# Optimization experiments

Hardware: AMD Instinct MI355X
Metric: run time of the kernel (lower is better)

Reference implementation:

```python
import jax, jax.numpy as jnp
import numpy as np

TOP_K = 2

def setup_inputs() -> dict:
    key = jax.random.key(0)
    k1, k2 = jax.random.split(key)
    hidden_states = jax.random.normal(k1, (4, 4096, 4096), dtype=jnp.float32)
    # nn.Linear(dim, num_experts, bias=False) weight: [num_experts, dim]
    router_weight = jax.random.normal(k2, (64, 4096), dtype=jnp.float32) * (4096 ** -0.5)
    return {"hidden_states": hidden_states, "router_weight": router_weight}

def reference(hidden_states, router_weight):
    # logits: (batch, seq, num_experts)
    logits = jnp.einsum('bsd,ed->bse', hidden_states, router_weight)
    # Shazeer et al. 2017 Eq. 1: softmax over the kept top-k logits.
    topk_logits, topk_indices = jax.lax.top_k(logits, TOP_K)
    topk_scores = jax.nn.softmax(topk_logits, axis=-1)  # (batch, seq, top_k)
    return topk_scores, topk_indices
```

## Files before the change

### kernel.cpp

```cpp
#include <hip/hip_runtime.h>
#include <math.h>

#define TOKENS 16384
#define DIM    4096
#define NEXP   64
#define KSPLIT 4
#define KSLICE (DIM / KSPLIT)
#define BK     32
#define NCHUNK (KSLICE / BK)
#define NCHUNK_G (DIM / BK)

typedef _Float16 f16x8 __attribute__((ext_vector_type(8)));
typedef float    f32x4 __attribute__((ext_vector_type(4)));

#define MFMA16(a, b, c) __builtin_amdgcn_mfma_f32_16x16x32_f16((a), (b), (c), 0, 0, 0)

__device__ __forceinline__ void gload16(const void* g, void* l) {
    __builtin_amdgcn_global_load_lds(
        (const __attribute__((address_space(1))) void*)g,
        (__attribute__((address_space(3))) void*)l, 16, 0, 0);
}

__global__ __launch_bounds__(256)
void pack_w_kernel(const float* __restrict__ w, uint4* __restrict__ wpk) {
    const int lane = threadIdx.x & 63;
    const int t    = threadIdx.x >> 6;
    const int c    = blockIdx.x;
    const int e    = 16 * t + (lane & 15);
    const int k0   = 32 * c + 8 * (lane >> 4);

    const float* src = w + (size_t)e * DIM + k0;
    const float4 v0 = *(const float4*)(src);
    const float4 v1 = *(const float4*)(src + 4);
    const float xs[8] = {v0.x, v0.y, v0.z, v0.w, v1.x, v1.y, v1.z, v1.w};

    f16x8 hi, lo;
#pragma unroll
    for (int j = 0; j < 8; ++j) {
        const float xv = xs[j];
        _Float16 h = (_Float16)xv;
        float hf = (float)h;
        if (fabsf(xv) < 6.103515625e-05f) {
            h = (_Float16)0.f; hf = 0.f;
        }
        hi[j] = h;
        lo[j] = (_Float16)((xv - hf) * 65536.f);
    }

    wpk[(size_t)c * 512 + (2 * t + 0) * 64 + lane] = *(const uint4*)&hi;
    wpk[(size_t)c * 512 + (2 * t + 1) * 64 + lane] = *(const uint4*)&lo;
}

__device__ __forceinline__ void split_a(const f32x4 lo, const f32x4 hi,
                                        f16x8& ah, f16x8& al) {
    const float xs[8] = {lo[0], lo[1], lo[2], lo[3], hi[0], hi[1], hi[2], hi[3]};
#pragma unroll
    for (int j = 0; j < 8; ++j) {
        const float xv = xs[j];
        const _Float16 h = (_Float16)xv;
        ah[j] = h;
        al[j] = (_Float16)((xv - (float)h) * 65536.f);
    }
}

__device__ __forceinline__ void fma3(const f16x8 ah, const f16x8 al,
                                     const f16x8 bh, const f16x8 bl,
                                     f32x4& a1, f32x4& a2) {
    a1 = MFMA16(ah, bh, a1);
    a2 = MFMA16(ah, bl, a2);
    a2 = MFMA16(al, bh, a2);
}

__global__ __launch_bounds__(256)
__attribute__((amdgpu_waves_per_eu(4, 4)))
void router_gemm_kernel(const float* __restrict__ x,
                        const uint4* __restrict__ wpk,
                        float* __restrict__ part) {
    __shared__ uint4 lds[2048];

    const int tid  = threadIdx.x;
    const int lane = tid & 63;
    const int wv   = tid >> 6;
    const int bid  = blockIdx.x;
    const int ks   = bid & (KSPLIT - 1);
    const int tb   = bid >> 2;
    const int wt0  = tb * 64 + wv * 16;

    const int rl = lane >> 3;
    const int sb = (lane & 7) ^ rl;
    const float* xsrc0 = x + (size_t)(wt0 + rl)     * DIM + ks * KSLICE + 4 * sb;
    const float* xsrc1 = x + (size_t)(wt0 + 8 + rl) * DIM + ks * KSLICE + 4 * sb;
    const uint4* bsrc = wpk + (size_t)(ks * NCHUNK) * 512 + (2 * wv) * 64 + lane;

    const int r  = lane & 15;
    const int kb = 2 * (lane >> 4);
    const int xi0 = r * 8 + ((kb    ) ^ (r & 7));
    const int xi1 = r * 8 + ((kb + 1) ^ (r & 7));

    f32x4 a10, a11, a12, a13, a20, a21, a22, a23;
    const f32x4 zero = {0.f, 0.f, 0.f, 0.f};
    a10 = a11 = a12 = a13 = zero;
    a20 = a21 = a22 = a23 = zero;

    auto STAGE = [&](int cc, int bsel) {
        uint4* Xb = &lds[bsel * 1024 + wv * 128];
        uint4* Bb = &lds[bsel * 1024 + 512 + (2 * wv) * 64];
        gload16(xsrc0 + cc * BK,            Xb);
        gload16(xsrc1 + cc * BK,            Xb + 64);
        gload16(bsrc + (size_t)cc * 512,      Bb);
        gload16(bsrc + (size_t)cc * 512 + 64, Bb + 64);
    };

    STAGE(0, 0);

#pragma unroll 1
    for (int c = 0; c < NCHUNK; ++c) {
        STAGE((c + 1) & (NCHUNK - 1), (c + 1) & 1);

        asm volatile("s_waitcnt vmcnt(4)" ::: "memory");
        __builtin_amdgcn_s_barrier();

        const uint4* Xr = &lds[(c & 1) * 1024 + wv * 128];
        const uint4* Br = &lds[(c & 1) * 1024 + 512];

        const f32x4 xlo = *(const f32x4*)&Xr[xi0];
        const f32x4 xhi = *(const f32x4*)&Xr[xi1];
        const f16x8 bh0 = *(const f16x8*)&Br[0 * 64 + lane];
        const f16x8 bl0 = *(const f16x8*)&Br[1 * 64 + lane];
        const f16x8 bh1 = *(const f16x8*)&Br[2 * 64 + lane];
        const f16x8 bl1 = *(const f16x8*)&Br[3 * 64 + lane];
        const f16x8 bh2 = *(const f16x8*)&Br[4 * 64 + lane];
        const f16x8 bl2 = *(const f16x8*)&Br[5 * 64 + lane];
        const f16x8 bh3 = *(const f16x8*)&Br[6 * 64 + lane];
        const f16x8 bl3 = *(const f16x8*)&Br[7 * 64 + lane];

        f16x8 ah, al;
        split_a(xlo, xhi, ah, al);
        fma3(ah, al, bh0, bl0, a10, a20);
        fma3(ah, al, bh1, bl1, a11, a21);
        fma3(ah, al, bh2, bl2, a12, a22);
        fma3(ah, al, bh3, bl3, a13, a23);

        asm volatile("s_waitcnt lgkmcnt(0)" ::: "memory");
        __builtin_amdgcn_s_barrier();
    }

    float* pout = part + ((size_t)ks * TOKENS + wt0 + 4 * (lane >> 4)) * NEXP
                + (lane & 15);
    const f32x4 v0 = a10 + a20 * (1.f / 65536.f);
    const f32x4 v1 = a11 + a21 * (1.f / 65536.f);
    const f32x4 v2 = a12 + a22 * (1.f / 65536.f);
    const f32x4 v3 = a13 + a23 * (1.f / 65536.f);
#pragma unroll
    for (int rr = 0; rr < 4; ++rr) {
        pout[(size_t)rr * NEXP +  0] = v0[rr];
        pout[(size_t)rr * NEXP + 16] = v1[rr];
        pout[(size_t)rr * NEXP + 32] = v2[rr];
        pout[(size_t)rr * NEXP + 48] = v3[rr];
    }
}

__global__ __launch_bounds__(256)
void topk_kernel(const float* __restrict__ part, float* __restrict__ out) {
    const int lane  = threadIdx.x & 63;
    const int wv    = threadIdx.x >> 6;
    const int token = blockIdx.x * 4 + wv;

    float logit = 0.f;
#pragma unroll
    for (int s = 0; s < KSPLIT; ++s)
        logit += part[((size_t)s * TOKENS + token) * NEXP + lane];

    float v1 = logit; int i1 = lane;
#pragma unroll
    for (int off = 32; off > 0; off >>= 1) {
        const float ov = __shfl_xor(v1, off);
        const int   oi = __shfl_xor(i1, off);
        if (ov > v1 || (ov == v1 && oi < i1)) { v1 = ov; i1 = oi; }
    }
    float v2 = (lane == i1) ? -INFINITY : logit; int i2 = lane;
#pragma unroll
    for (int off = 32; off > 0; off >>= 1) {
        const float ov = __shfl_xor(v2, off);
        const int   oi = __shfl_xor(i2, off);
        if (ov > v2 || (ov == v2 && oi < i2)) { v2 = ov; i2 = oi; }
    }

    if (lane == 0) {
        const float e = expf(v2 - v1);
        const float r = 1.f / (1.f + e);
        out[2 * token + 0] = r;
        out[2 * token + 1] = e * r;
        out[2 * TOKENS + 2 * token + 0] = (float)i1;
        out[2 * TOKENS + 2 * token + 1] = (float)i2;
    }
}

extern "C" void kernel_launch(void* const* d_in, const int* in_sizes, int n_in,
                              void* d_out, int out_size, void* d_ws, size_t ws_size,
                              hipStream_t stream) {
    const float* x = (const float*)d_in[0];
    const float* w = (const float*)d_in[1];
    float* out  = (float*)d_out;
    float* part = (float*)d_ws;
    uint4* wpk = (uint4*)((char*)d_ws + (size_t)KSPLIT * TOKENS * NEXP * sizeof(float));

    pack_w_kernel<<<NCHUNK_G, 256, 0, stream>>>(w, wpk);
    router_gemm_kernel<<<(TOKENS / 64) * KSPLIT, 256, 0, stream>>>(x, wpk, part);
    topk_kernel<<<TOKENS / 4, 256, 0, stream>>>(part, out);
}
```

Before: 380.3 us.

## Load activations directly to registers and stage weights in 8-chunk LDS blocks

The router GEMM no longer routes activation tiles through LDS. Each lane loads its fp32 activations straight into registers, with a software pipeline that prefetches two chunks ahead. Weight tiles are staged into LDS eight K-chunks at a time, so a barrier is needed only once per eight chunks instead of twice per chunk. Blocks grow to 512 threads covering 128 tokens, the waves-per-EU attribute is removed, and sched_barriers pin the ordering of loads and MFMAs. The intent is to cut barrier and LDS round-trip overhead on this memory-bound kernel, at the cost of more registers and exposed latency whenever a weight block is restaged.

Measured after the change: 393.1 us. 1.03x slower.

```diff
diff --git a/kernel.cpp b/kernel.cpp
--- a/kernel.cpp
+++ b/kernel.cpp
@@ -8,12 +8,15 @@
 #define KSLICE (DIM / KSPLIT)
 #define BK     32
 #define NCHUNK (KSLICE / BK)
+#define QCHUNK 8
+#define TB     128
 #define NCHUNK_G (DIM / BK)
 
 typedef _Float16 f16x8 __attribute__((ext_vector_type(8)));
 typedef float    f32x4 __attribute__((ext_vector_type(4)));
 
 #define MFMA16(a, b, c) __builtin_amdgcn_mfma_f32_16x16x32_f16((a), (b), (c), 0, 0, 0)
+#define SBAR() __builtin_amdgcn_sched_barrier(0)
 
 __device__ __forceinline__ void gload16(const void* g, void* l) {
     __builtin_amdgcn_global_load_lds(
@@ -51,9 +54,9 @@
     wpk[(size_t)c * 512 + (2 * t + 1) * 64 + lane] = *(const uint4*)&lo;
 }
 
-__device__ __forceinline__ void split_a(const f32x4 lo, const f32x4 hi,
+__device__ __forceinline__ void split_a(const float4 lo, const float4 hi,
                                         f16x8& ah, f16x8& al) {
-    const float xs[8] = {lo[0], lo[1], lo[2], lo[3], hi[0], hi[1], hi[2], hi[3]};
+    const float xs[8] = {lo.x, lo.y, lo.z, lo.w, hi.x, hi.y, hi.z, hi.w};
 #pragma unroll
     for (int j = 0; j < 8; ++j) {
         const float xv = xs[j];
@@ -71,78 +74,85 @@
     a2 = MFMA16(al, bh, a2);
 }
 
-__global__ __launch_bounds__(256)
-__attribute__((amdgpu_waves_per_eu(4, 4)))
+__global__ __launch_bounds__(512)
 void router_gemm_kernel(const float* __restrict__ x,
                         const uint4* __restrict__ wpk,
                         float* __restrict__ part) {
-    __shared__ uint4 lds[2048];
+    __shared__ uint4 Blds[QCHUNK * 512];
 
     const int tid  = threadIdx.x;
     const int lane = tid & 63;
     const int wv   = tid >> 6;
     const int bid  = blockIdx.x;
     const int ks   = bid & (KSPLIT - 1);
-    const int tb   = bid >> 2;
-    const int wt0  = tb * 64 + wv * 16;
-
-    const int rl = lane >> 3;
-    const int sb = (lane & 7) ^ rl;
-    const float* xsrc0 = x + (size_t)(wt0 + rl)     * DIM + ks * KSLICE + 4 * sb;
-    const float* xsrc1 = x + (size_t)(wt0 + 8 + rl) * DIM + ks * KSLICE + 4 * sb;
-    const uint4* bsrc = wpk + (size_t)(ks * NCHUNK) * 512 + (2 * wv) * 64 + lane;
-
-    const int r  = lane & 15;
-    const int kb = 2 * (lane >> 4);
-    const int xi0 = r * 8 + ((kb    ) ^ (r & 7));
-    const int xi1 = r * 8 + ((kb + 1) ^ (r & 7));
+    const int wt0  = (bid >> 2) * TB + wv * 16;
+
+    const float* xp = x + (size_t)(wt0 + (lane & 15)) * DIM
+                    + ks * KSLICE + 8 * (lane >> 4);
+
+    const uint4* bsl = wpk + (size_t)ks * NCHUNK * 512 + (size_t)(wv * 8) * 64 + lane;
+
+    auto STAGE_B = [&](int q) {
+        const uint4* src = bsl + (size_t)q * QCHUNK * 512;
+#pragma unroll
+        for (int i = 0; i < 8; ++i)
+            gload16(src + i * 64, &Blds[(wv * 8 + i) * 64]);
+    };
 
     f32x4 a10, a11, a12, a13, a20, a21, a22, a23;
     const f32x4 zero = {0.f, 0.f, 0.f, 0.f};
     a10 = a11 = a12 = a13 = zero;
     a20 = a21 = a22 = a23 = zero;
 
-    auto STAGE = [&](int cc, int bsel) {
-        uint4* Xb = &lds[bsel * 1024 + wv * 128];
-        uint4* Bb = &lds[bsel * 1024 + 512 + (2 * wv) * 64];
-        gload16(xsrc0 + cc * BK,            Xb);
-        gload16(xsrc1 + cc * BK,            Xb + 64);
-        gload16(bsrc + (size_t)cc * 512,      Bb);
-        gload16(bsrc + (size_t)cc * 512 + 64, Bb + 64);
-    };
-
-    STAGE(0, 0);
+    float4 rl[4], rh[4];
+
+    STAGE_B(0);
+    rl[0] = *(const float4*)(xp);
+    rh[0] = *(const float4*)(xp + 4);
+    rl[1] = *(const float4*)(xp + BK);
+    rh[1] = *(const float4*)(xp + BK + 4);
+    asm volatile("s_waitcnt vmcnt(0)" ::: "memory");
+    __builtin_amdgcn_s_barrier();
 
 #pragma unroll 1
-    for (int c = 0; c < NCHUNK; ++c) {
-        STAGE((c + 1) & (NCHUNK - 1), (c + 1) & 1);
-
-        asm volatile("s_waitcnt vmcnt(4)" ::: "memory");
-        __builtin_amdgcn_s_barrier();
-
-        const uint4* Xr = &lds[(c & 1) * 1024 + wv * 128];
-        const uint4* Br = &lds[(c & 1) * 1024 + 512];
-
-        const f32x4 xlo = *(const f32x4*)&Xr[xi0];
-        const f32x4 xhi = *(const f32x4*)&Xr[xi1];
-        const f16x8 bh0 = *(const f16x8*)&Br[0 * 64 + lane];
-        const f16x8 bl0 = *(const f16x8*)&Br[1 * 64 + lane];
-        const f16x8 bh1 = *(const f16x8*)&Br[2 * 64 + lane];
-        const f16x8 bl1 = *(const f16x8*)&Br[3 * 64 + lane];
-        const f16x8 bh2 = *(const f16x8*)&Br[4 * 64 + lane];
-        const f16x8 bl2 = *(const f16x8*)&Br[5 * 64 + lane];
-        const f16x8 bh3 = *(const f16x8*)&Br[6 * 64 + lane];
-        const f16x8 bl3 = *(const f16x8*)&Br[7 * 64 + lane];
-
-        f16x8 ah, al;
-        split_a(xlo, xhi, ah, al);
-        fma3(ah, al, bh0, bl0, a10, a20);
-        fma3(ah, al, bh1, bl1, a11, a21);
-        fma3(ah, al, bh2, bl2, a12, a22);
-        fma3(ah, al, bh3, bl3, a13, a23);
-
-        asm volatile("s_waitcnt lgkmcnt(0)" ::: "memory");
-        __builtin_amdgcn_s_barrier();
+    for (int c = 0; c < NCHUNK; c += 4) {
+        if (c && (c & (QCHUNK - 1)) == 0) {
+            asm volatile("s_waitcnt lgkmcnt(0)" ::: "memory");
+            __builtin_amdgcn_s_barrier();
+            STAGE_B(c >> 3);
+            asm volatile("s_waitcnt vmcnt(0)" ::: "memory");
+            __builtin_amdgcn_s_barrier();
+        }
+#pragma unroll
+        for (int u = 0; u < 4; ++u) {
+            const int cc = c + u;
+            SBAR();
+            {
+                const int cn = (cc + 2) & (NCHUNK - 1);
+                rl[(u + 2) & 3] = *(const float4*)(xp + cn * BK);
+                rh[(u + 2) & 3] = *(const float4*)(xp + cn * BK + 4);
+            }
+            SBAR();
+            const uint4* Br = &Blds[((cc & (QCHUNK - 1)) * 8) * 64];
+            f16x8 ah, al;
+            split_a(rl[u], rh[u], ah, al);
+            {
+                const f16x8 bh0 = *(const f16x8*)&Br[0 * 64 + lane];
+                const f16x8 bl0 = *(const f16x8*)&Br[1 * 64 + lane];
+                const f16x8 bh1 = *(const f16x8*)&Br[2 * 64 + lane];
+                const f16x8 bl1 = *(const f16x8*)&Br[3 * 64 + lane];
+                fma3(ah, al, bh0, bl0, a10, a20);
+                fma3(ah, al, bh1, bl1, a11, a21);
+            }
+            {
+                const f16x8 bh2 = *(const f16x8*)&Br[4 * 64 + lane];
+                const f16x8 bl2 = *(const f16x8*)&Br[5 * 64 + lane];
+                const f16x8 bh3 = *(const f16x8*)&Br[6 * 64 + lane];
+                const f16x8 bl3 = *(const f16x8*)&Br[7 * 64 + lane];
+                fma3(ah, al, bh2, bl2, a12, a22);
+                fma3(ah, al, bh3, bl3, a13, a23);
+            }
+        }
     }
 
     float* pout = part + ((size_t)ks * TOKENS + wt0 + 4 * (lane >> 4)) * NEXP
@@ -206,6 +216,6 @@
     uint4* wpk = (uint4*)((char*)d_ws + (size_t)KSPLIT * TOKENS * NEXP * sizeof(float));
 
     pack_w_kernel<<<NCHUNK_G, 256, 0, stream>>>(w, wpk);
-    router_gemm_kernel<<<(TOKENS / 64) * KSPLIT, 256, 0, stream>>>(x, wpk, part);
+    router_gemm_kernel<<<(TOKENS / TB) * KSPLIT, 512, 0, stream>>>(x, wpk, part);
     topk_kernel<<<TOKENS / 4, 256, 0, stream>>>(part, out);
 }
```

## Enlarge GEMM block to 128 tokens with 2x2 wave tiling and deeper X prefetch

Applied to the files above, without the earlier changes.

The router GEMM block grows from 256 to 512 threads and covers 128 tokens. Each wave now computes a 32-token by 32-expert tile, so the f16 hi/lo split of activations is shared across two expert tiles and each weight fragment is reused across two token tiles. X is prefetched two chunks ahead into a 4-deep LDS ring, and MFMA priority is raised with s_setprio. The aim is to cut redundant split work and hide global load latency better. The cost is more LDS, more registers per wave, and half as many blocks, which may hurt occupancy and load balance.

Result: no change. 385.2 us (+1.3%).

```diff
diff --git a/kernel.cpp b/kernel.cpp
--- a/kernel.cpp
+++ b/kernel.cpp
@@ -8,6 +8,7 @@
 #define KSLICE (DIM / KSPLIT)
 #define BK     32
 #define NCHUNK (KSLICE / BK)
+#define TB     128
 #define NCHUNK_G (DIM / BK)
 
 typedef _Float16 f16x8 __attribute__((ext_vector_type(8)));
@@ -71,92 +72,109 @@
     a2 = MFMA16(al, bh, a2);
 }
 
-__global__ __launch_bounds__(256)
+__global__ __launch_bounds__(512)
 __attribute__((amdgpu_waves_per_eu(4, 4)))
 void router_gemm_kernel(const float* __restrict__ x,
                         const uint4* __restrict__ wpk,
                         float* __restrict__ part) {
-    __shared__ uint4 lds[2048];
+    __shared__ uint4 lds[5120];
 
     const int tid  = threadIdx.x;
     const int lane = tid & 63;
     const int wv   = tid >> 6;
+    const int tf   = wv >> 1;
+    const int et   = wv & 1;
     const int bid  = blockIdx.x;
     const int ks   = bid & (KSPLIT - 1);
-    const int tb   = bid >> 2;
-    const int wt0  = tb * 64 + wv * 16;
+    const int token0 = (bid >> 2) * TB;
 
     const int rl = lane >> 3;
     const int sb = (lane & 7) ^ rl;
-    const float* xsrc0 = x + (size_t)(wt0 + rl)     * DIM + ks * KSLICE + 4 * sb;
-    const float* xsrc1 = x + (size_t)(wt0 + 8 + rl) * DIM + ks * KSLICE + 4 * sb;
-    const uint4* bsrc = wpk + (size_t)(ks * NCHUNK) * 512 + (2 * wv) * 64 + lane;
-
-    const int r  = lane & 15;
-    const int kb = 2 * (lane >> 4);
-    const int xi0 = r * 8 + ((kb    ) ^ (r & 7));
-    const int xi1 = r * 8 + ((kb + 1) ^ (r & 7));
-
-    f32x4 a10, a11, a12, a13, a20, a21, a22, a23;
+    const float* xsrc0 = x + (size_t)(token0 + 16 * wv + rl) * DIM
+                       + ks * KSLICE + 4 * sb;
+    const float* xsrc1 = xsrc0 + (size_t)8 * DIM;
+    const uint4* bsrc = wpk + (size_t)(ks * NCHUNK) * 512 + wv * 64 + lane;
+
+    const int xib = ((lane >> 3) & 1) * 64 + (lane & 7) * 8;
+    const int xk0 = (2 * (lane >> 4)    ) ^ (lane & 7);
+    const int xk1 = (2 * (lane >> 4) + 1) ^ (lane & 7);
+
+    f32x4 a1[2][2], a2[2][2];
     const f32x4 zero = {0.f, 0.f, 0.f, 0.f};
-    a10 = a11 = a12 = a13 = zero;
-    a20 = a21 = a22 = a23 = zero;
-
-    auto STAGE = [&](int cc, int bsel) {
-        uint4* Xb = &lds[bsel * 1024 + wv * 128];
-        uint4* Bb = &lds[bsel * 1024 + 512 + (2 * wv) * 64];
-        gload16(xsrc0 + cc * BK,            Xb);
-        gload16(xsrc1 + cc * BK,            Xb + 64);
-        gload16(bsrc + (size_t)cc * 512,      Bb);
-        gload16(bsrc + (size_t)cc * 512 + 64, Bb + 64);
-    };
-
-    STAGE(0, 0);
+#pragma unroll
+    for (int f = 0; f < 2; ++f)
+#pragma unroll
+        for (int e = 0; e < 2; ++e) { a1[f][e] = zero; a2[f][e] = zero; }
+
+    gload16(xsrc0,          &lds[0 * 1024 + wv * 128]);
+    gload16(xsrc0 + BK,     &lds[1 * 1024 + wv * 128]);
+    gload16(xsrc1,          &lds[0 * 1024 + wv * 128 + 64]);
+    gload16(xsrc1 + BK,     &lds[1 * 1024 + wv * 128 + 64]);
+    gload16(bsrc,           &lds[4096 + 0 * 512 + wv * 64]);
 
 #pragma unroll 1
     for (int c = 0; c < NCHUNK; ++c) {
-        STAGE((c + 1) & (NCHUNK - 1), (c + 1) & 1);
-
-        asm volatile("s_waitcnt vmcnt(4)" ::: "memory");
+        {
+            const int cb = (c + 1) & (NCHUNK - 1);
+            gload16(bsrc + (size_t)cb * 512,
+                    &lds[4096 + ((c + 1) & 1) * 512 + wv * 64]);
+        }
+        if (!(c & 1)) {
+            const int c2 = (c + 2) & (NCHUNK - 1);
+            const int c3 = (c + 3) & (NCHUNK - 1);
+            uint4* d2 = &lds[((c + 2) & 3) * 1024 + wv * 128];
+            uint4* d3 = &lds[((c + 3) & 3) * 1024 + wv * 128];
+            gload16(xsrc0 + c2 * BK, d2);
+            gload16(xsrc0 + c3 * BK, d3);
+            gload16(xsrc1 + c2 * BK, d2 + 64);
+            gload16(xsrc1 + c3 * BK, d3 + 64);
+        }
+        asm volatile("s_waitcnt vmcnt(5)" ::: "memory");
         __builtin_amdgcn_s_barrier();
 
-        const uint4* Xr = &lds[(c & 1) * 1024 + wv * 128];
-        const uint4* Br = &lds[(c & 1) * 1024 + 512];
-
-        const f32x4 xlo = *(const f32x4*)&Xr[xi0];
-        const f32x4 xhi = *(const f32x4*)&Xr[xi1];
-        const f16x8 bh0 = *(const f16x8*)&Br[0 * 64 + lane];
-        const f16x8 bl0 = *(const f16x8*)&Br[1 * 64 + lane];
-        const f16x8 bh1 = *(const f16x8*)&Br[2 * 64 + lane];
-        const f16x8 bl1 = *(const f16x8*)&Br[3 * 64 + lane];
-        const f16x8 bh2 = *(const f16x8*)&Br[4 * 64 + lane];
-        const f16x8 bl2 = *(const f16x8*)&Br[5 * 64 + lane];
-        const f16x8 bh3 = *(const f16x8*)&Br[6 * 64 + lane];
-        const f16x8 bl3 = *(const f16x8*)&Br[7 * 64 + lane];
-
-        f16x8 ah, al;
-        split_a(xlo, xhi, ah, al);
-        fma3(ah, al, bh0, bl0, a10, a20);
-        fma3(ah, al, bh1, bl1, a11, a21);
-        fma3(ah, al, bh2, bl2, a12, a22);
-        fma3(ah, al, bh3, bl3, a13, a23);
+        const uint4* Xr = &lds[(c & 3) * 1024];
+        const uint4* Br = &lds[4096 + (c & 1) * 512];
+
+        f16x8 ah0, al0, ah1, al1;
+        {
+            const int b0 = (2 * tf + 0) * 128 + xib;
+            const int b1 = (2 * tf + 1) * 128 + xib;
+            const f32x4 A0l = *(const f32x4*)&Xr[b0 + xk0];
+            const f32x4 A0h = *(const f32x4*)&Xr[b0 + xk1];
+            const f32x4 A1l = *(const f32x4*)&Xr[b1 + xk0];
+            const f32x4 A1h = *(const f32x4*)&Xr[b1 + xk1];
+            split_a(A0l, A0h, ah0, al0);
+            split_a(A1l, A1h, ah1, al1);
+        }
+        const f16x8 bh0 = *(const f16x8*)&Br[(4 * et + 0) * 64 + lane];
+        const f16x8 bl0 = *(const f16x8*)&Br[(4 * et + 1) * 64 + lane];
+        const f16x8 bh1 = *(const f16x8*)&Br[(4 * et + 2) * 64 + lane];
+        const f16x8 bl1 = *(const f16x8*)&Br[(4 * et + 3) * 64 + lane];
+
+        __builtin_amdgcn_s_setprio(1);
+        fma3(ah0, al0, bh0, bl0, a1[0][0], a2[0][0]);
+        fma3(ah0, al0, bh1, bl1, a1[0][1], a2[0][1]);
+        fma3(ah1, al1, bh0, bl0, a1[1][0], a2[1][0]);
+        fma3(ah1, al1, bh1, bl1, a1[1][1], a2[1][1]);
+        __builtin_amdgcn_s_setprio(0);
 
         asm volatile("s_waitcnt lgkmcnt(0)" ::: "memory");
         __builtin_amdgcn_s_barrier();
     }
 
-    float* pout = part + ((size_t)ks * TOKENS + wt0 + 4 * (lane >> 4)) * NEXP
-                + (lane & 15);
-    const f32x4 v0 = a10 + a20 * (1.f / 65536.f);
-    const f32x4 v1 = a11 + a21 * (1.f / 65536.f);
-    const f32x4 v2 = a12 + a22 * (1.f / 65536.f);
-    const f32x4 v3 = a13 + a23 * (1.f / 65536.f);
-#pragma unroll
-    for (int rr = 0; rr < 4; ++rr) {
-        pout[(size_t)rr * NEXP +  0] = v0[rr];
-        pout[(size_t)rr * NEXP + 16] = v1[rr];
-        pout[(size_t)rr * NEXP + 32] = v2[rr];
-        pout[(size_t)rr * NEXP + 48] = v3[rr];
+#pragma unroll
+    for (int f = 0; f < 2; ++f) {
+#pragma unroll
+        for (int e = 0; e < 2; ++e) {
+            const f32x4 v = a1[f][e] + a2[f][e] * (1.f / 65536.f);
+            float* pout = part
+                + ((size_t)ks * TOKENS + token0 + (2 * tf + f) * 16
+                   + 4 * (lane >> 4)) * NEXP
+                + 16 * (2 * et + e) + (lane & 15);
+#pragma unroll
+            for (int rr = 0; rr < 4; ++rr)
+                pout[(size_t)rr * NEXP] = v[rr];
+        }
     }
 }
 
@@ -206,6 +224,6 @@
     uint4* wpk = (uint4*)((char*)d_ws + (size_t)KSPLIT * TOKENS * NEXP * sizeof(float));
 
     pack_w_kernel<<<NCHUNK_G, 256, 0, stream>>>(w, wpk);
-    router_gemm_kernel<<<(TOKENS / 64) * KSPLIT, 256, 0, stream>>>(x, wpk, part);
+    router_gemm_kernel<<<(TOKENS / TB) * KSPLIT, 512, 0, stream>>>(x, wpk, part);
     topk_kernel<<<TOKENS / 4, 256, 0, stream>>>(part, out);
 }
```
